# Performance work log

Measured on AMD Instinct MI355X. Metric: run time of the kernel, lower is better.

Reference implementation:

```python
import jax, jax.numpy as jnp
import numpy as np

N, D = 8192, 64

def setup_inputs() -> dict:
    key = jax.random.key(0)
    sentence = jax.random.uniform(key, (N, D), dtype=jnp.float32)
    return {"sentence": sentence}

def reference(sentence):
    # weights[i, j] = <sentence[i], sentence[j]>  -> [n, n]
    weights = jnp.einsum('id,jd->ij', sentence, sentence)
    # sum-normalize each row (NOT softmax)
    weights = weights / jnp.sum(weights, axis=1, keepdims=True)
    # reweighted vectors: [n, n] @ [n, d] -> [n, d]
    return jnp.matmul(weights, sentence)
```

## Files before the change

kernel.cpp:

```cpp
#include <hip/hip_runtime.h>

#define N 8192
#define D 64
#define P 64
#define SLICE (D * D + D)
#define SLICE4 (SLICE / 4)

__global__ __launch_bounds__(256) void gram_partial(const float* __restrict__ S,
                                                    float* __restrict__ ws) {
    const int tid = threadIdx.x;
    const int ty = tid >> 4;
    const int tx = tid & 15;

    float acc[4][4];
#pragma unroll
    for (int i = 0; i < 4; ++i)
#pragma unroll
        for (int j = 0; j < 4; ++j) acc[i][j] = 0.f;
    float tac[4] = {0.f, 0.f, 0.f, 0.f};

    const int rpb = N / P;
    const int r0 = blockIdx.x * rpb;
    const float* Sa = S + (size_t)r0 * D + 4 * ty;
    const float* Sb = S + (size_t)r0 * D + 4 * tx;

#pragma unroll 8
    for (int r = 0; r < rpb; ++r) {
        const float4 a = *(const float4*)(Sa + (size_t)r * D);
        const float4 b = *(const float4*)(Sb + (size_t)r * D);
        const float av[4] = {a.x, a.y, a.z, a.w};
        const float bv[4] = {b.x, b.y, b.z, b.w};
#pragma unroll
        for (int i = 0; i < 4; ++i)
#pragma unroll
            for (int j = 0; j < 4; ++j) acc[i][j] += av[i] * bv[j];
        if (ty == 0) {
#pragma unroll
            for (int j = 0; j < 4; ++j) tac[j] += bv[j];
        }
    }

    float* pw = ws + (size_t)blockIdx.x * SLICE;
#pragma unroll
    for (int i = 0; i < 4; ++i)
        *(float4*)(pw + (4 * ty + i) * D + 4 * tx) =
            make_float4(acc[i][0], acc[i][1], acc[i][2], acc[i][3]);
    if (ty == 0)
        *(float4*)(pw + D * D + 4 * tx) =
            make_float4(tac[0], tac[1], tac[2], tac[3]);
}

__global__ __launch_bounds__(256) void reduce_kernel(float* __restrict__ ws) {
    const float4* src = (const float4*)ws;
    float4* dst = (float4*)(ws + (size_t)P * SLICE);
    const int gid = blockIdx.x * 256 + threadIdx.x;
    for (int i4 = gid; i4 < SLICE4; i4 += 1024) {
        float4 acc = make_float4(0.f, 0.f, 0.f, 0.f);
#pragma unroll 8
        for (int p = 0; p < P; ++p) {
            const float4 v = src[(size_t)p * SLICE4 + i4];
            acc.x += v.x; acc.y += v.y; acc.z += v.z; acc.w += v.w;
        }
        dst[i4] = acc;
    }
}

__global__ __launch_bounds__(256) void apply_kernel(const float* __restrict__ S,
                                                    const float* __restrict__ G,
                                                    const float* __restrict__ t,
                                                    float* __restrict__ out) {
    __shared__ float Gs[D * D];
    __shared__ float ts[D];
    const int tid = threadIdx.x;
#pragma unroll
    for (int i = tid; i < (D * D) / 4; i += 256)
        ((float4*)Gs)[i] = ((const float4*)G)[i];
    if (tid < D) ts[tid] = t[tid];
    __syncthreads();

    const int lane = tid & 63;
    const int wid = tid >> 6;
    const float tl = ts[lane];

    const int ia = (blockIdx.x * 4 + wid) * 2;
    const int ib = ia + 1;
    const float va = S[(size_t)ia * D + lane];
    const float vb = S[(size_t)ib * D + lane];

    float pa = va * tl, pb = vb * tl;
#pragma unroll
    for (int s = 1; s < 64; s <<= 1) {
        pa += __shfl_xor(pa, s, 64);
        pb += __shfl_xor(pb, s, 64);
    }

    float aa = 0.f, ab = 0.f;
#pragma unroll
    for (int k = 0; k < D; ++k) {
        const float g = Gs[k * D + lane];
        aa += __shfl(va, k, 64) * g;
        ab += __shfl(vb, k, 64) * g;
    }
    out[(size_t)ia * D + lane] = aa / pa;
    out[(size_t)ib * D + lane] = ab / pb;
}

extern "C" void kernel_launch(void* const* d_in, const int* in_sizes, int n_in,
                              void* d_out, int out_size, void* d_ws, size_t ws_size,
                              hipStream_t stream) {
    const float* S = (const float*)d_in[0];
    float* out = (float*)d_out;
    float* ws = (float*)d_ws;
    float* Gfin = ws + (size_t)P * SLICE;
    float* tfin = Gfin + D * D;

    gram_partial<<<P, 256, 0, stream>>>(S, ws);
    reduce_kernel<<<4, 256, 0, stream>>>(ws);
    apply_kernel<<<1024, 256, 0, stream>>>(S, Gfin, tfin, out);
}
```

Baseline: 85.12 us.

## Fuse gram, reduce and apply stages into one cooperative kernel with grid syncs

Replaces the three-kernel pipeline (partial Gram, reduction, apply) with a single cooperative kernel of 256 blocks. Two grid-wide syncs separate the stages. The partial Gram work is spread over more blocks. The reduction is parallelised across waves, with lane-level loads followed by shuffle reductions instead of a 4-block serial loop over partials. The goal is to remove inter-kernel launch gaps and the serial reduction bottleneck, at the cost of grid-sync overhead and a dependence on every block being co-resident. The original three-kernel path is kept as a fallback if the cooperative launch fails.

New measurement: 183.8 us. 116% more time.

```diff
diff --git a/kernel.cpp b/kernel.cpp
--- a/kernel.cpp
+++ b/kernel.cpp
@@ -1,10 +1,132 @@
 #include <hip/hip_runtime.h>
+#include <hip/hip_cooperative_groups.h>
+
+namespace cg = cooperative_groups;
 
 #define N 8192
 #define D 64
-#define P 64
+#define NB 256
 #define SLICE (D * D + D)
 #define SLICE4 (SLICE / 4)
+#define PF 64
+
+__global__ __launch_bounds__(256) void fused_kernel(const float* __restrict__ S,
+                                                    float* __restrict__ ws,
+                                                    float* __restrict__ out) {
+    cg::grid_group grid = cg::this_grid();
+    const int tid = threadIdx.x;
+    const int bid = blockIdx.x;
+
+    {
+        const int ty = tid >> 4;
+        const int tx = tid & 15;
+        float acc[4][4];
+#pragma unroll
+        for (int i = 0; i < 4; ++i)
+#pragma unroll
+            for (int j = 0; j < 4; ++j) acc[i][j] = 0.f;
+        float tac[4] = {0.f, 0.f, 0.f, 0.f};
+
+        const int rpb = N / NB;
+        const float* Sa = S + (size_t)(bid * rpb) * D + 4 * ty;
+        const float* Sb = S + (size_t)(bid * rpb) * D + 4 * tx;
+#pragma unroll 8
+        for (int r = 0; r < rpb; ++r) {
+            const float4 a = *(const float4*)(Sa + (size_t)r * D);
+            const float4 b = *(const float4*)(Sb + (size_t)r * D);
+            const float av[4] = {a.x, a.y, a.z, a.w};
+            const float bv[4] = {b.x, b.y, b.z, b.w};
+#pragma unroll
+            for (int i = 0; i < 4; ++i)
+#pragma unroll
+                for (int j = 0; j < 4; ++j) acc[i][j] += av[i] * bv[j];
+            if (ty == 0) {
+#pragma unroll
+                for (int j = 0; j < 4; ++j) tac[j] += bv[j];
+            }
+        }
+        float* pw = ws + (size_t)bid * SLICE;
+#pragma unroll
+        for (int i = 0; i < 4; ++i)
+            *(float4*)(pw + (4 * ty + i) * D + 4 * tx) =
+                make_float4(acc[i][0], acc[i][1], acc[i][2], acc[i][3]);
+        if (ty == 0)
+            *(float4*)(pw + D * D + 4 * tx) =
+                make_float4(tac[0], tac[1], tac[2], tac[3]);
+    }
+    __threadfence();
+    grid.sync();
+
+    {
+        const float4* src = (const float4*)ws;
+        float4* dst = (float4*)(ws + (size_t)NB * SLICE);
+        const int w = tid >> 6;
+        const int lane = tid & 63;
+        const int wc0 = bid * 4 + w;
+
+#pragma unroll
+        for (int e = 0; e < 2; ++e) {
+            const int wc = e ? (1024 + wc0) : wc0;
+            if (e && wc0 >= 16) break;
+            float4 acc = make_float4(0.f, 0.f, 0.f, 0.f);
+#pragma unroll
+            for (int q = 0; q < 4; ++q) {
+                const float4 v = src[(size_t)(4 * lane + q) * SLICE4 + wc];
+                acc.x += v.x; acc.y += v.y; acc.z += v.z; acc.w += v.w;
+            }
+#pragma unroll
+            for (int s = 1; s < 64; s <<= 1) {
+                acc.x += __shfl_xor(acc.x, s, 64);
+                acc.y += __shfl_xor(acc.y, s, 64);
+                acc.z += __shfl_xor(acc.z, s, 64);
+                acc.w += __shfl_xor(acc.w, s, 64);
+            }
+            if (lane == 0) dst[wc] = acc;
+        }
+    }
+    __threadfence();
+    grid.sync();
+
+    {
+        __shared__ float Gs[D * D];
+        __shared__ float ts[D];
+        const float* Gf = ws + (size_t)NB * SLICE;
+#pragma unroll
+        for (int i = tid; i < (D * D) / 4; i += 256)
+            ((float4*)Gs)[i] = ((const float4*)Gf)[i];
+        if (tid < D) ts[tid] = Gf[D * D + tid];
+        __syncthreads();
+
+        const int lane = tid & 63;
+        const int w = tid >> 6;
+        const float tl = ts[lane];
+
+#pragma unroll
+        for (int p = 0; p < 4; ++p) {
+            const int ia = bid * 32 + w * 8 + 2 * p;
+            const int ib = ia + 1;
+            const float va = S[(size_t)ia * D + lane];
+            const float vb = S[(size_t)ib * D + lane];
+
+            float pa = va * tl, pb = vb * tl;
+#pragma unroll
+            for (int s = 1; s < 64; s <<= 1) {
+                pa += __shfl_xor(pa, s, 64);
+                pb += __shfl_xor(pb, s, 64);
+            }
+
+            float aa = 0.f, ab = 0.f;
+#pragma unroll
+            for (int k = 0; k < D; ++k) {
+                const float g = Gs[k * D + lane];
+                aa += __shfl(va, k, 64) * g;
+                ab += __shfl(vb, k, 64) * g;
+            }
+            out[(size_t)ia * D + lane] = aa / pa;
+            out[(size_t)ib * D + lane] = ab / pb;
+        }
+    }
+}
 
 __global__ __launch_bounds__(256) void gram_partial(const float* __restrict__ S,
                                                     float* __restrict__ ws) {
@@ -19,7 +141,7 @@
         for (int j = 0; j < 4; ++j) acc[i][j] = 0.f;
     float tac[4] = {0.f, 0.f, 0.f, 0.f};
 
-    const int rpb = N / P;
+    const int rpb = N / PF;
     const int r0 = blockIdx.x * rpb;
     const float* Sa = S + (size_t)r0 * D + 4 * ty;
     const float* Sb = S + (size_t)r0 * D + 4 * tx;
@@ -52,12 +174,12 @@
 
 __global__ __launch_bounds__(256) void reduce_kernel(float* __restrict__ ws) {
     const float4* src = (const float4*)ws;
-    float4* dst = (float4*)(ws + (size_t)P * SLICE);
+    float4* dst = (float4*)(ws + (size_t)NB * SLICE);
     const int gid = blockIdx.x * 256 + threadIdx.x;
     for (int i4 = gid; i4 < SLICE4; i4 += 1024) {
         float4 acc = make_float4(0.f, 0.f, 0.f, 0.f);
 #pragma unroll 8
-        for (int p = 0; p < P; ++p) {
+        for (int p = 0; p < PF; ++p) {
             const float4 v = src[(size_t)p * SLICE4 + i4];
             acc.x += v.x; acc.y += v.y; acc.z += v.z; acc.w += v.w;
         }
@@ -111,10 +233,17 @@
     const float* S = (const float*)d_in[0];
     float* out = (float*)d_out;
     float* ws = (float*)d_ws;
-    float* Gfin = ws + (size_t)P * SLICE;
+    float* Gfin = ws + (size_t)NB * SLICE;
     float* tfin = Gfin + D * D;
 
-    gram_partial<<<P, 256, 0, stream>>>(S, ws);
-    reduce_kernel<<<4, 256, 0, stream>>>(ws);
-    apply_kernel<<<1024, 256, 0, stream>>>(S, Gfin, tfin, out);
-}
+    void* args[] = {(void*)&S, (void*)&ws, (void*)&out};
+    hipError_t err = hipLaunchCooperativeKernel((const void*)fused_kernel,
+                                                dim3(NB), dim3(256), args, 0,
+                                                stream);
+    if (err != hipSuccess) {
+        (void)hipGetLastError();
+        gram_partial<<<PF, 256, 0, stream>>>(S, ws);
+        reduce_kernel<<<4, 256, 0, stream>>>(ws);
+        apply_kernel<<<1024, 256, 0, stream>>>(S, Gfin, tfin, out);
+    }
+}
```
